# Optimization experiments

Measured on AMD Instinct MI355X. Metric: run time of the kernel, lower is better.

The kernel has to match this reference:

```python
import jax, jax.numpy as jnp
import numpy as np

H, W, V = 32, 64, 13
B, C_IN = 8, 256
RADIUS = 6371.0 * 1000.0
NUM_LAT = H + 2
_j = np.arange(1, NUM_LAT - 1, dtype=np.float64)
_LATS = (90.0 - _j * 180.0 / (NUM_LAT - 1)) * np.pi / 180.0  # [32] radians
PIXEL_X = jnp.asarray(2.0 * np.pi * RADIUS * np.cos(_LATS) / W, dtype=jnp.float32).reshape(1, 1, H, 1)
PIXEL_Y = np.float32(np.pi * RADIUS / (H + 1))
_DZ = np.array([50, 50, 50, 50, 50, 75, 100, 100, 100, 125, 112, 75, 75], dtype=np.float32)
PIXEL_Z = jnp.asarray(_DZ).reshape(1, V, 1, 1)
PRESSURE = jnp.asarray([50, 100, 150, 200, 250, 300, 400, 500, 600, 700, 850, 925, 1000], dtype=jnp.float32).reshape(1, V, 1, 1)
M_Z = jnp.asarray(np.tril(np.ones((V, V), dtype=np.float32)) * _DZ[None, :])  # lower-tri integration matrix
LAT_GRID = jnp.asarray(_LATS, dtype=jnp.float32).reshape(1, 1, H, 1)

OMEGA, L_V, R_GAS, C_P, R_D = 7.29e-5, 2.5e6, 8.314, 1005.0, 287.0
DIFF_RATIO, DT, K_H, K_V = 0.05, 300.0, 15.0, 0.1
SIGMA, EMIS, PTHRESH = 5.67e-8, 0.7, 0.8
sg = jax.lax.stop_gradient


def d_x(f):  # periodic 4th-order diff along W, kernel [1,-8,0,8,-1]/12
    g = (jnp.roll(f, 2, 3) - 8.0 * jnp.roll(f, 1, 3) + 8.0 * jnp.roll(f, -1, 3) - jnp.roll(f, -2, 3)) / 12.0
    return g / PIXEL_X


def d_y(f):  # replicate-block padding along H, kernel [-1,8,0,-8,1]/12
    p = jnp.concatenate([f[:, :, :2], f, f[:, :, -2:]], axis=2)
    g = (-p[:, :, :-4] + 8.0 * p[:, :, 1:-3] - 8.0 * p[:, :, 3:-1] + p[:, :, 4:]) / 12.0
    return g / PIXEL_Y


def d_z(f):  # replicate-block padding along level dim (axis 1)
    p = jnp.concatenate([f[:, :2], f, f[:, -2:]], axis=1)
    g = (-p[:, :-4] + 8.0 * p[:, 1:-3] - 8.0 * p[:, 3:-1] + p[:, 4:]) / 12.0
    return g / PIXEL_Z


def integral_z(f):
    return jnp.einsum('ij,bjhw->bihw', M_Z, f)


def conv3x3(x, w, b):
    y = jax.lax.conv_general_dilated(x, w, (1, 1), ((1, 1), (1, 1)), dimension_numbers=('NCHW', 'OIHW', 'NCHW'))
    return y + b[None, :, None, None]


def batchnorm(x, g, b, eps=1e-5):  # training-mode BN (batch statistics)
    m = x.mean(axis=(0, 2, 3), keepdims=True)
    v = x.var(axis=(0, 2, 3), keepdims=True)
    return (x - m) / jnp.sqrt(v + eps) * g.reshape(1, -1, 1, 1) + b.reshape(1, -1, 1, 1)


def scale_tensor(t, a, b):
    mn, mx = sg(t.min()), sg(t.max())
    return (t - mn) / (mx - mn) * (b - a) + a


def scale_diff(d, x):
    mn, me, mx = sg(x.min()), sg(x.mean()), sg(x.max())
    return scale_tensor(d, (mn - me) * DIFF_RATIO, (mx - me) * DIFF_RATIO)


def avoid_inf(t, thr=1.0):
    t = jnp.where(jnp.abs(t) == 0.0, jnp.full_like(t, 0.1), t)
    return jnp.where(jnp.abs(t) < thr, jnp.sign(t) * thr, t)


def mixing(f):
    return K_H * (d_x(d_x(f)) + d_y(d_y(f))) + K_V * d_z(d_z(f))


def rad_cool(t):
    ta = t + 273.15
    return -(EMIS * SIGMA * ta ** 4) / (C_P * PRESSURE * 100.0 / (R_D * ta))


def saturation(t, z_z):
    rho = -1.0 / avoid_inf(z_z)
    p = rho * R_GAS * t
    tc = t - 273.15
    e_s = 6.112 * jnp.exp(scale_tensor(17.67 * tc / avoid_inf(tc + 243.5), -3.47, 3.01)) * 100.0
    return jnp.maximum(0.622 * e_s / avoid_inf(p - 0.378 * e_s), 1e-6)


def precip(q, q_s):
    rh = q / avoid_inf(q_s)
    rate = (rh > PTHRESH).astype(q.dtype) * (q - PTHRESH * q_s) / DT
    return rate, rate * L_V / C_P


def uv_dt(u, v, w, u_x, v_y, z_x, z_y):
    # u_x, v_y are held fixed across RK stages (stateful self.u_x/self.v_y in the original)
    f_cor = 2.0 * OMEGA * jnp.sin(LAT_GRID)
    u_t = -u * u_x - v * d_y(u) - w * d_z(u) + f_cor * v - z_x + mixing(u)
    v_t = -u * d_x(v) - v * v_y - w * d_z(v) - f_cor * u - z_y + mixing(v)
    return u_t, v_t


def t_dt(u, v, w, t, q, q_s, z_z):
    Q = -L_V * z_z * w
    _, lh = precip(q, q_s)
    return (Q - z_z * w) / C_P - u * d_x(t) - v * d_y(t) - w * d_z(t) + mixing(t) + rad_cool(t) + lh


def pde_forward(x, w_norm, b_norm, w_innorm, b_innorm, coef, gz, bz, gq, bq, gu, bu, gv, bv, gt, bt, gblk, bblk):
    h = conv3x3(x, w_norm, b_norm)  # [B, 65, H, W]
    z, q, u, v, t = jnp.split(h, 5, axis=1)
    z = batchnorm(z, gz, bz); q = batchnorm(q, gq, bq)
    u = batchnorm(u, gu, bu); v = batchnorm(v, gv, bv); t = batchnorm(t, gt, bt)
    z_x, z_y, z_z = d_x(z), d_y(z), d_z(z)
    u_x, v_y = d_x(u), d_y(v)
    w_vel = -integral_z(u_x + v_y)  # continuity: dw/dz = -(u_x + v_y)
    # --- RK4 momentum evolution ---
    k1u, k1v = uv_dt(u, v, w_vel, u_x, v_y, z_x, z_y)
    k2u, k2v = uv_dt(u + 0.5 * DT * k1u, v + 0.5 * DT * k1v, w_vel, u_x, v_y, z_x, z_y)
    k3u, k3v = uv_dt(u + 0.5 * DT * k2u, v + 0.5 * DT * k2v, w_vel, u_x, v_y, z_x, z_y)
    k4u, k4v = uv_dt(u + DT * k3u, v + DT * k3v, w_vel, u_x, v_y, z_x, z_y)
    u_new = u + sg(scale_diff((k1u + 2 * k2u + 2 * k3u + k4u) / 6.0 * DT, u))
    v_new = v + sg(scale_diff((k1v + 2 * k2v + 2 * k3v + k4v) / 6.0 * DT, v))
    # --- RK4 temperature evolution (q_s fixed from initial t) ---
    q_s = saturation(t, z_z)
    k1t = t_dt(u, v, w_vel, t, q, q_s, z_z)
    k2t = t_dt(u, v, w_vel, t + 0.5 * DT * k1t, q, q_s, z_z)
    k3t = t_dt(u, v, w_vel, t + 0.5 * DT * k2t, q, q_s, z_z)
    k4t = t_dt(u, v, w_vel, t + DT * k3t, q, q_s, z_z)
    t_new = t + sg(scale_diff((k1t + 2 * k2t + 2 * k3t + k4t) / 6.0 * DT, t))
    # geopotential tendency uses stateful self.t_t (last computed stage = k4t)
    z_t = integral_z(-R_GAS / PRESSURE * k4t)
    z_new = z + sg(scale_diff(z_t * DT, z))
    # moisture evolution
    pr, _ = precip(q, q_s)
    q_t = -u * d_x(q) - v * d_y(q) - w_vel * d_z(q) + mixing(q) - pr
    q_new = q + sg(scale_diff(q_t * DT, q))
    phys = jnp.concatenate([z_new, q_new, u_new, v_new, t_new], axis=1)
    out = coef * phys + (1.0 - coef) * h
    out = conv3x3(out, w_innorm, b_innorm)
    return batchnorm(out, gblk, bblk) + x


def setup_inputs() -> dict:
    key = jax.random.key(0)
    k0, k1, k2 = jax.random.split(key, 3)
    VD = V * 5
    ones13 = jnp.ones((V,), jnp.float32)
    zeros13 = jnp.zeros((V,), jnp.float32)
    return {
        'x': jax.random.normal(k0, (B, C_IN, H, W), jnp.float32),
        'w_norm': jax.random.normal(k1, (VD, C_IN, 3, 3), jnp.float32) * 0.02,
        'b_norm': jnp.zeros((VD,), jnp.float32),
        'w_innorm': jax.random.normal(k2, (C_IN, VD, 3, 3), jnp.float32) * 0.02,
        'b_innorm': jnp.zeros((C_IN,), jnp.float32),
        'coef': 0.5 * jnp.ones((1, VD, H, W), jnp.float32),
        'gz': 0.1 * ones13, 'bz': zeros13,
        'gq': 0.1 * ones13, 'bq': zeros13,
        'gu': 0.1 * ones13, 'bu': zeros13,
        'gv': 0.1 * ones13, 'bv': zeros13,
        'gt': 0.1 * ones13, 'bt': zeros13,
        'gblk': jnp.ones((C_IN,), jnp.float32),
        'bblk': jnp.zeros((C_IN,), jnp.float32),
    }


def reference(x, w_norm, b_norm, w_innorm, b_innorm, coef, gz, bz, gq, bq, gu, bu, gv, bv, gt, bt, gblk, bblk):
    return pde_forward(x, w_norm, b_norm, w_innorm, b_innorm, coef, gz, bz, gq, bq, gu, bu, gv, bv, gt, bt, gblk, bblk)
```

## Files before the change

### kernel.cpp

```cpp
#include <hip/hip_runtime.h>
#include <math.h>

#define DEVFN static __device__ __forceinline__

static constexpr int BB = 8, VV = 13, HH = 32, WW = 64;
static constexpr int NPLANE = HH * WW;
static constexpr int NF = BB * VV * NPLANE;
static constexpr int NHB = BB * 65 * NPLANE;

static constexpr float DT = 300.0f;
static constexpr float KHc = 15.0f, KVc = 0.1f;
static constexpr float OMEGAc = 7.29e-5f;
static constexpr float L_Vc = 2.5e6f;
static constexpr float R_GASc = 8.314f;
static constexpr float C_Pc = 1005.0f;
static constexpr float PTHc = 0.8f;
static constexpr float PYc  = (float)(3.14159265358979323846 * 6371000.0 / 33.0);
static constexpr float PXCc = (float)(2.0 * 3.14159265358979323846 * 6371000.0 / 64.0);
static constexpr float RCCc = (float)(0.7 * 5.67e-8 * 287.0 / (1005.0 * 100.0));
static constexpr float FBIG = 3.402823466e38f;

__constant__ float cDZ[13]  = {50,50,50,50,50,75,100,100,100,125,112,75,75};
__constant__ float cPRS[13] = {50,100,150,200,250,300,400,500,600,700,850,925,1000};

typedef short bf16x8 __attribute__((ext_vector_type(8)));
typedef float f32x4 __attribute__((ext_vector_type(4)));

DEVFN int pmh(int r){ return r < 0 ? r + 2 : (r > HH - 1 ? r - 2 : r); }
DEVFN int pmv(int r){ return r < 0 ? r + 2 : (r > VV - 1 ? r - 2 : r); }
DEVFN float latOf(int h){ return (90.0f - (float)(h + 1) * (180.0f / 33.0f)) * 0.017453292519943295f; }
DEVFN float avoid_inf(float t){
  if (t == 0.0f) t = 0.1f;
  if (fabsf(t) < 1.0f) t = copysignf(1.0f, t);
  return t;
}
DEVFN unsigned short f2bf(float f){
  unsigned u = __float_as_uint(f);
  unsigned r = (u + 0x7fffu + ((u >> 16) & 1u)) >> 16;
  return (unsigned short)r;
}

DEVFN float d_xf(const float* __restrict__ F, int rb, int w, float invpx){
  return (F[rb + ((w + 62) & 63)] - 8.f * F[rb + ((w + 63) & 63)]
        + 8.f * F[rb + ((w + 1) & 63)] - F[rb + ((w + 2) & 63)]) * (1.f / 12.f) * invpx;
}
DEVFN float d_yf(const float* __restrict__ F, int bvbase, int h, int w){
  return (-F[bvbase + pmh(h - 2) * 64 + w] + 8.f * F[bvbase + pmh(h - 1) * 64 + w]
          - 8.f * F[bvbase + pmh(h + 1) * 64 + w] + F[bvbase + pmh(h + 2) * 64 + w]) * (1.f / 12.f) * (1.f / PYc);
}
DEVFN float d_zf(const float* __restrict__ F, int bbase, int v, int hw){
  return (-F[bbase + pmv(v - 2) * 2048 + hw] + 8.f * F[bbase + pmv(v - 1) * 2048 + hw]
          - 8.f * F[bbase + pmv(v + 1) * 2048 + hw] + F[bbase + pmv(v + 2) * 2048 + hw]) * (1.f / 12.f) / cDZ[v];
}
DEVFN float dxxf(const float* __restrict__ F, int rb, int w, float invpx){
  float s = F[rb + ((w + 60) & 63)] - 16.f * F[rb + ((w + 61) & 63)] + 64.f * F[rb + ((w + 62) & 63)]
          + 16.f * F[rb + ((w + 63) & 63)] - 130.f * F[rb + w] + 16.f * F[rb + ((w + 1) & 63)]
          + 64.f * F[rb + ((w + 2) & 63)] - 16.f * F[rb + ((w + 3) & 63)] + F[rb + ((w + 4) & 63)];
  return s * (1.f / 144.f) * invpx * invpx;
}
DEVFN float dyyf(const float* __restrict__ F, int bvbase, int h, int w){
  float g0 = d_yf(F, bvbase, pmh(h - 2), w);
  float g1 = d_yf(F, bvbase, pmh(h - 1), w);
  float g2 = d_yf(F, bvbase, pmh(h + 1), w);
  float g3 = d_yf(F, bvbase, pmh(h + 2), w);
  return (-g0 + 8.f * g1 - 8.f * g2 + g3) * (1.f / 12.f) * (1.f / PYc);
}
DEVFN float dzzf(const float* __restrict__ F, int bbase, int v, int hw){
  float g0 = d_zf(F, bbase, pmv(v - 2), hw);
  float g1 = d_zf(F, bbase, pmv(v - 1), hw);
  float g2 = d_zf(F, bbase, pmv(v + 1), hw);
  float g3 = d_zf(F, bbase, pmv(v + 2), hw);
  return (-g0 + 8.f * g1 - 8.f * g2 + g3) * (1.f / 12.f) / cDZ[v];
}

DEVFN float waveRedSum(float v){ for (int o = 32; o; o >>= 1) v += __shfl_down(v, o, 64); return v; }
DEVFN float waveRedMin(float v){ for (int o = 32; o; o >>= 1) v = fminf(v, __shfl_down(v, o, 64)); return v; }
DEVFN float waveRedMax(float v){ for (int o = 32; o; o >>= 1) v = fmaxf(v, __shfl_down(v, o, 64)); return v; }

template<int OP, int NWV>
static __device__ float blockRedN(float v){
  __shared__ float s[NWV];
  v = OP == 0 ? waveRedSum(v) : OP == 1 ? waveRedMin(v) : waveRedMax(v);
  int lane = threadIdx.x & 63, wid = threadIdx.x >> 6;
  __syncthreads();
  if (lane == 0) s[wid] = v;
  __syncthreads();
  float r = s[0];
  #pragma unroll
  for (int k = 1; k < NWV; ++k)
    r = OP == 0 ? r + s[k] : OP == 1 ? fminf(r, s[k]) : fmaxf(r, s[k]);
  return r;
}

struct GB { const float* g[5]; const float* b[5]; };

__global__ void __launch_bounds__(256) pre_k(const float* __restrict__ x,
    const float* __restrict__ w1, const float* __restrict__ w2,
    unsigned short* __restrict__ XT, unsigned short* __restrict__ wp1,
    unsigned short* __restrict__ wp2)
{
  int blk = blockIdx.x, t = threadIdx.x;
  if (blk < 1024){
    __shared__ float tile[16 * 68];
    int zz = blk >> 8, rem = blk & 255;
    int b = rem >> 5, h = rem & 31;
    for (int p = zz * 4; p < zz * 4 + 4; ++p){
      int cbase = p * 16;
      __syncthreads();
      {
        int cl = t >> 4, w4 = (t & 15) * 4;
        float4 v = *(const float4*)(x + (((size_t)(b * 256 + cbase + cl) * 32 + h) * 64 + w4));
        tile[cl * 68 + w4 + 0] = v.x; tile[cl * 68 + w4 + 1] = v.y;
        tile[cl * 68 + w4 + 2] = v.z; tile[cl * 68 + w4 + 3] = v.w;
      }
      __syncthreads();
      {
        int w = t >> 2, c4 = (t & 3) * 4;
        ushort4 o;
        o.x = f2bf(tile[(c4 + 0) * 68 + w]);
        o.y = f2bf(tile[(c4 + 1) * 68 + w]);
        o.z = f2bf(tile[(c4 + 2) * 68 + w]);
        o.w = f2bf(tile[(c4 + 3) * 68 + w]);
        *(ushort4*)(XT + (((size_t)(b * 32 + h) * 64 + w) * 256 + cbase + c4)) = o;
      }
    }
  } else {
    const int T1 = 9 * 80 * 256;
    const int T2 = 9 * 256 * 96;
    int idx = (blk - 1024) * 256 + t;
    if (idx < T1){
      int dir = idx / (80 * 256);
      int r = idx - dir * (80 * 256);
      int co = r / 256, ci = r - co * 256;
      float v = (co < 65) ? w1[((size_t)(co * 256 + ci)) * 9 + dir] : 0.f;
      wp1[idx] = f2bf(v);
    } else if (idx < T1 + T2){
      int j = idx - T1;
      int dir = j / (256 * 96);
      int r = j - dir * (256 * 96);
      int co = r / 96, ci = r - co * 96;
      float v = (ci < 65) ? w2[((size_t)(co * 65 + ci)) * 9 + dir] : 0.f;
      wp2[j] = f2bf(v);
    }
  }
}

template<int CIT, int CIL, int CO, int COp, int NW, int MF, int SWZ>
__global__ void __launch_bounds__(NW * 64) conv_mfma_k(
    const unsigned short* __restrict__ XT, const unsigned short* __restrict__ Wp,
    const float* __restrict__ bias, float* __restrict__ out, float* __restrict__ bnp)
{
  __shared__ __align__(16) unsigned short Xl[3 * 34 * CIL];
  const int C8 = CIL / 8;
  int tid = threadIdx.x;
// ... 102 lines not shown
        float g = gb.g[f][k], bbv = gb.b[f][k];
        As[ch] = g * rstd; Bs[ch] = bbv - m * g * rstd;
      }
    }
  }
  __syncthreads();

  int part = blk >> 6;
  int col = ((blk & 63) << 8) | t;
  int b = col >> 11, p = col & 2047, h = p >> 6, w = p & 63;
  int hbase = b * 65 * NPLANE;
  auto hn = [&](int ch, int hh, int ww)->float {
    return hb[hbase + ch * 2048 + hh * 64 + ww] * As[ch] + Bs[ch];
  };
  int fb = (b * 13) * 2048 + p;
  float lat = latOf(h);
  float invpx = 1.0f / (PXCc * cosf(lat));
  int wm2 = (w + 62) & 63, wm1 = (w + 63) & 63, wpl1 = (w + 1) & 63, wpl2 = (w + 2) & 63;
  int hm2 = pmh(h - 2), hm1 = pmh(h - 1), hp1 = pmh(h + 1), hp2 = pmh(h + 2);
  float fmn = FBIG, fmx = -FBIG, fsm = 0.f, smn = FBIG, smx = -FBIG;
  if (part < 5){
    int ch0 = part * 13;
    float c[13];
    #pragma unroll
    for (int v = 0; v < 13; ++v) c[v] = hn(ch0 + v, h, w);
    float* Fdst = part == 0 ? Fz : part == 1 ? Fq : part == 2 ? Fu : part == 3 ? Fvf : Ft;
    #pragma unroll
    for (int v = 0; v < 13; ++v) Fdst[fb + v * 2048] = c[v];
    if (part == 0){
      #pragma unroll
      for (int v = 0; v < 13; ++v){
        zz[fb + v * 2048] = (-c[pmv(v - 2)] + 8.f * c[pmv(v - 1)] - 8.f * c[pmv(v + 1)] + c[pmv(v + 2)]) * (1.f / 12.f) / cDZ[v];
        float zxv = (hn(v, h, wm2) - 8.f * hn(v, h, wm1) + 8.f * hn(v, h, wpl1) - hn(v, h, wpl2)) * (1.f / 12.f) * invpx;
        float zyv = (-hn(v, hm2, w) + 8.f * hn(v, hm1, w) - 8.f * hn(v, hp1, w) + hn(v, hp2, w)) * (1.f / 12.f) * (1.f / PYc);
        zx[fb + v * 2048] = zxv; zy[fb + v * 2048] = zyv;
      }
    }
    if (part == 2){
      #pragma unroll
      for (int v = 0; v < 13; ++v){
        float uxv = (hn(26 + v, h, wm2) - 8.f * hn(26 + v, h, wm1) + 8.f * hn(26 + v, h, wpl1) - hn(26 + v, h, wpl2)) * (1.f / 12.f) * invpx;
        ux[fb + v * 2048] = uxv;
      }
    }
    if (part == 3){
      #pragma unroll
      for (int v = 0; v < 13; ++v){
        float vyv = (-hn(39 + v, hm2, w) + 8.f * hn(39 + v, hm1, w) - 8.f * hn(39 + v, hp1, w) + hn(39 + v, hp2, w)) * (1.f / 12.f) * (1.f / PYc);
        vy[fb + v * 2048] = vyv;
      }
    }
    if (part == 4){
      #pragma unroll
      for (int v = 0; v < 13; ++v){
        float tcc = c[v] - 273.15f;
        float arg = 17.67f * tcc / avoid_inf(tcc + 243.5f);
        smn = fminf(smn, arg); smx = fmaxf(smx, arg);
      }
    }
    #pragma unroll
    for (int v = 0; v < 13; ++v){ fmn = fminf(fmn, c[v]); fmx = fmaxf(fmx, c[v]); fsm += c[v]; }
  } else {
    float cum = 0.f;
    #pragma unroll
    for (int v = 0; v < 13; ++v){
      float uxv = (hn(26 + v, h, wm2) - 8.f * hn(26 + v, h, wm1) + 8.f * hn(26 + v, h, wpl1) - hn(26 + v, h, wpl2)) * (1.f / 12.f) * invpx;
      float vyv = (-hn(39 + v, hm2, w) + 8.f * hn(39 + v, hm1, w) - 8.f * hn(39 + v, hp1, w) + hn(39 + v, hp2, w)) * (1.f / 12.f) * (1.f / PYc);
      cum += cDZ[v] * (uxv + vyv);
      wv[fb + v * 2048] = -cum;
    }
  }
  float* pb = partS + blk * 17;
  float r;
  r = blockRedN<1,4>(smn); if (!t) pb[0] = r;
  r = blockRedN<2,4>(smx); if (!t) pb[1] = r;
  #pragma unroll
  for (int f = 0; f < 5; ++f){
    r = blockRedN<1,4>(part == f ? fmn : FBIG);  if (!t) pb[2 + f * 3] = r;
    r = blockRedN<2,4>(part == f ? fmx : -FBIG); if (!t) pb[3 + f * 3] = r;
    r = blockRedN<0,4>(part == f ? fsm : 0.f);   if (!t) pb[4 + f * 3] = r;
  }
}

template<int STAGE>
__global__ void __launch_bounds__(256) stage_k(
  const float* U, const float* Vf, const float* T,
  const float* Fu, const float* Fvf, const float* Ft, const float* Fq,
  const float* ux, const float* vy, const float* zx, const float* zy,
  const float* wv, const float* zz, const float* partS,
  float* C0, float* prr,
  float* Uo, float* Vo, float* To,
  float* duA, float* dvA, float* dtA, float* k4t, float* qtA,
  float* pduv, float* pdt, float* pqt, float cnext)
{
  float ss = 0.f, off = 0.f;
  if (STAGE == 1){
    int tt = threadIdx.x;
    float v0 = partS[tt * 17], v1 = partS[tt * 17 + 1];
    if (tt < 128){
      v0 = fminf(v0, partS[(tt + 256) * 17]);
      v1 = fmaxf(v1, partS[(tt + 256) * 17 + 1]);
    }
    float smn = blockRedN<1,4>(v0);
    float smx = blockRedN<2,4>(v1);
    ss = (3.01f + 3.47f) / (smx - smn);
    off = -3.47f - smn * ss;
  }
  int i = blockIdx.x * 256 + threadIdx.x;
  int w = i & 63, h = (i >> 6) & 31;
  int bv = i >> 11;
  int v = bv % 13;
  int bvbase = bv * 2048;
  int rb = bvbase + h * 64;
  int bbase = (bv - v) * 2048;
  int hw = h * 64 + w;
  float lat = latOf(h);
  float invpx = 1.0f / (PXCc * cosf(lat));
  float fcor = 2.0f * OMEGAc * sinf(lat);
  float wvi = wv[i];
  float Ui = U[i], Vi = Vf[i], Ti = T[i];
  float Fui = (STAGE == 1) ? Ui : Fu[i];
  float Fvi = (STAGE == 1) ? Vi : Fvf[i];

  float dyU = d_yf(U, bvbase, h, w);
  float dzU = d_zf(U, bbase, v, hw);
  float dxV = d_xf(Vf, rb, w, invpx);
  float dzV = d_zf(Vf, bbase, v, hw);
  float mixU = KHc * (dxxf(U, rb, w, invpx) + dyyf(U, bvbase, h, w)) + KVc * dzzf(U, bbase, v, hw);
  float mixV = KHc * (dxxf(Vf, rb, w, invpx) + dyyf(Vf, bvbase, h, w)) + KVc * dzzf(Vf, bbase, v, hw);
  float ku = -Ui * ux[i] - Vi * dyU - wvi * dzU + fcor * Vi - zx[i] + mixU;
  float kv = -Ui * dxV - Vi * vy[i] - wvi * dzV - fcor * Ui - zy[i] + mixV;

  float C0i;
  if (STAGE == 1){
    float zzi = zz[i], qi = Fq[i];
    float rho = -1.0f / avoid_inf(zzi);
    float p = rho * R_GASc * Ti;
    float tcc = Ti - 273.15f;
    float arg = 17.67f * tcc / avoid_inf(tcc + 243.5f);
    float es = 6.112f * expf(arg * ss + off) * 100.0f;
    float qs = fmaxf(0.622f * es / avoid_inf(p - 0.378f * es), 1e-6f);
    float rh = qi / avoid_inf(qs);
    float rate = (rh > PTHc) ? (qi - PTHc * qs) * (1.0f / DT) : 0.0f;
    prr[i] = rate;
    C0i = -(L_Vc + 1.0f) * zzi * wvi * (1.0f / C_Pc) + rate * (L_Vc / C_Pc);
    C0[i] = C0i;
  } else {
    C0i = C0[i];
  }

  float dxT = d_xf(T, rb, w, invpx);
  float dyT = d_yf(T, bvbase, h, w);
  float dzT = d_zf(T, bbase, v, hw);
  float mixT = KHc * (dxxf(T, rb, w, invpx) + dyyf(T, bvbase, h, w)) + KVc * dzzf(T, bbase, v, hw);
  float ta = Ti + 273.15f;
  float t2 = ta * ta;
  float ta5 = t2 * t2 * ta;
  float rc = -RCCc * ta5 / cPRS[v];
  float kt = C0i - Fui * dxT - Fvi * dyT - wvi * dzT + mixT + rc;

  if (STAGE == 1){ duA[i] = ku; dvA[i] = kv; dtA[i] = kt; }
  else if (STAGE < 4){ duA[i] += 2.f * ku; dvA[i] += 2.f * kv; dtA[i] += 2.f * kt; }
  else {
    float au = duA[i] + ku, av = dvA[i] + kv, at = dtA[i] + kt;
    duA[i] = au; dvA[i] = av; dtA[i] = at; k4t[i] = kt;
    float m0 = blockRedN<1,4>(au), m1 = blockRedN<2,4>(au);
    float m2 = blockRedN<1,4>(av), m3 = blockRedN<2,4>(av);
    float m4 = blockRedN<1,4>(at), m5 = blockRedN<2,4>(at);
    if (!threadIdx.x){
      float* pp = pduv + blockIdx.x * 4;
      pp[0] = m0; pp[1] = m1; pp[2] = m2; pp[3] = m3;
      pdt[blockIdx.x * 2] = m4; pdt[blockIdx.x * 2 + 1] = m5;
    }
  }
  if (STAGE < 4){
    float Fti = (STAGE == 1) ? Ti : Ft[i];
    Uo[i] = Fui + cnext * ku;
    Vo[i] = Fvi + cnext * kv;
    To[i] = Fti + cnext * kt;
  }

  if (STAGE == 2){
    float qtv = -Fui * d_xf(Fq, rb, w, invpx) - Fvi * d_yf(Fq, bvbase, h, w) - wvi * d_zf(Fq, bbase, v, hw)
              + KHc * (dxxf(Fq, rb, w, invpx) + dyyf(Fq, bvbase, h, w)) + KVc * dzzf(Fq, bbase, v, hw) - prr[i];
    qtA[i] = qtv;
    float m0 = blockRedN<1,4>(qtv), m1 = blockRedN<2,4>(qtv);
    if (!threadIdx.x){ pqt[blockIdx.x * 2] = m0; pqt[blockIdx.x * 2 + 1] = m1; }
  }
}

__global__ void __launch_bounds__(64) zt_k(const float* __restrict__ k4t, float* __restrict__ zt, float* __restrict__ pmm)
{
  int col = blockIdx.x * 64 + threadIdx.x;
  int b = col >> 11, p = col & 2047;
  int fb = b * 13 * 2048 + p;
  float cum = 0.f, mn = FBIG, mx = -FBIG;
  #pragma unroll
  for (int v = 0; v < 13; ++v){
    cum += cDZ[v] * (-R_GASc / cPRS[v]) * k4t[fb + v * 2048];
    zt[fb + v * 2048] = cum;
    mn = fminf(mn, cum); mx = fmaxf(mx, cum);
  }
  mn = waveRedMin(mn); mx = waveRedMax(mx);
  if (!threadIdx.x){ pmm[blockIdx.x * 2] = mn; pmm[blockIdx.x * 2 + 1] = mx; }
}

__global__ void __launch_bounds__(256) outmid_fused_k(
  const float* __restrict__ hb,
  const float* __restrict__ Fz, const float* __restrict__ Fq, const float* __restrict__ Fu,
  const float* __restrict__ Fvf, const float* __restrict__ Ft,
  const float* __restrict__ ztA, const float* __restrict__ qtA,
  const float* __restrict__ duA, const float* __restrict__ dvA, const float* __restrict__ dtA,
  const float* __restrict__ coef, const float* __restrict__ partS,
  const float* __restrict__ pduv, const float* __restrict__ pdt,
  const float* __restrict__ pqt, const float* __restrict__ pzt,
  unsigned short* __restrict__ MT)
{
  __shared__ float tileBig[65 * 66];
  int blk = blockIdx.x, t = threadIdx.x;

  float fmn[5] = {FBIG, FBIG, FBIG, FBIG, FBIG};
  float fmx[5] = {-FBIG, -FBIG, -FBIG, -FBIG, -FBIG};
  float fsm[5] = {0.f, 0.f, 0.f, 0.f, 0.f};
  #pragma unroll 1
  for (int r0 = t; r0 < 384; r0 += 256){
    const float* pr = partS + r0 * 17;
    #pragma unroll
    for (int f = 0; f < 5; ++f){
      fmn[f] = fminf(fmn[f], pr[2 + f * 3]);
      fmx[f] = fmaxf(fmx[f], pr[3 + f * 3]);
      fsm[f] += pr[4 + f * 3];
    }
  }
  #pragma unroll
  for (int f = 0; f < 5; ++f){
    fmn[f] = blockRedN<1,4>(fmn[f]);
    fmx[f] = blockRedN<2,4>(fmx[f]);
    fsm[f] = blockRedN<0,4>(fsm[f]);
  }
  float dumn = FBIG, dumx = -FBIG, dvmn = FBIG, dvmx = -FBIG, dtmn = FBIG, dtmx = -FBIG;
  float qmn = FBIG, qmx = -FBIG;
  #pragma unroll 1
  for (int r0 = t; r0 < 832; r0 += 256){
    dumn = fminf(dumn, pduv[r0 * 4]);     dumx = fmaxf(dumx, pduv[r0 * 4 + 1]);
    dvmn = fminf(dvmn, pduv[r0 * 4 + 2]); dvmx = fmaxf(dvmx, pduv[r0 * 4 + 3]);
    dtmn = fminf(dtmn, pdt[r0 * 2]);      dtmx = fmaxf(dtmx, pdt[r0 * 2 + 1]);
    qmn = fminf(qmn, pqt[r0 * 2]);        qmx = fmaxf(qmx, pqt[r0 * 2 + 1]);
  }
  float zmn = pzt[t * 2], zmx = pzt[t * 2 + 1];
  dumn = blockRedN<1,4>(dumn); dumx = blockRedN<2,4>(dumx);
  dvmn = blockRedN<1,4>(dvmn); dvmx = blockRedN<2,4>(dvmx);
  dtmn = blockRedN<1,4>(dtmn); dtmx = blockRedN<2,4>(dtmx);
  qmn = blockRedN<1,4>(qmn);   qmx = blockRedN<2,4>(qmx);
  zmn = blockRedN<1,4>(zmn);   zmx = blockRedN<2,4>(zmx);

  float scf[5], off2[5];
  {
    float rmn[5] = {zmn, qmn, dumn, dvmn, dtmn};
    float rmx[5] = {zmx, qmx, dumx, dvmx, dtmx};
    float cfs[5] = {DT, DT, DT / 6.f, DT / 6.f, DT / 6.f};
    #pragma unroll
    for (int f = 0; f < 5; ++f){
      float mnf = fmn[f], mef = fsm[f] * (1.0f / (float)NF), mxf = fmx[f];
      float aa = (mnf - mef) * 0.05f, b2 = (mxf - mef) * 0.05f;
      float cf = cfs[f];
      float dmn = rmn[f] * cf, dmx = rmx[f] * cf;
      float s = (b2 - aa) / (dmx - dmn);
      scf[f] = s * cf; off2[f] = aa - dmn * s;
    }
  }

  int b = blk >> 5, h = blk & 31;
  #pragma unroll 1
  for (int idx = t; idx < 65 * 64; idx += 256){
    int c = idx >> 6, w = idx & 63;
    int f = c / 13, v = c - f * 13;
    int fi = (b * 13 + v) * 2048 + h * 64 + w;
    const float *Fp, *Rp;
    switch (f){
      case 0: Fp = Fz;  Rp = ztA; break;
      case 1: Fp = Fq;  Rp = qtA; break;
      case 2: Fp = Fu;  Rp = duA; break;
      case 3: Fp = Fvf; Rp = dvA; break;
      default: Fp = Ft; Rp = dtA; break;
    }
    float phys = Fp[fi] + Rp[fi] * scf[f] + off2[f];
    float cf = coef[c * 2048 + h * 64 + w];
    float hbv = hb[((size_t)(b * 65 + c)) * 2048 + h * 64 + w];
    tileBig[c * 66 + w] = cf * phys + (1.0f - cf) * hbv;
  }
  __syncthreads();
  #pragma unroll 1
  for (int ph = 0; ph < 6; ++ph){
    int cbase = ph * 16;
    int w = t >> 2, c4 = (t & 3) * 4;
    int c0 = cbase + c4;
    ushort4 o;
    o.x = (c0 + 0 < 65) ? f2bf(tileBig[(c0 + 0) * 66 + w]) : (unsigned short)0;
    o.y = (c0 + 1 < 65) ? f2bf(tileBig[(c0 + 1) * 66 + w]) : (unsigned short)0;
    o.z = (c0 + 2 < 65) ? f2bf(tileBig[(c0 + 2) * 66 + w]) : (unsigned short)0;
    o.w = (c0 + 3 < 65) ? f2bf(tileBig[(c0 + 3) * 66 + w]) : (unsigned short)0;
    *(ushort4*)(MT + (((size_t)(b * 32 + h) * 64 + w) * 96 + c0)) = o;
  }
}

__global__ void __launch_bounds__(256) final_k(float* __restrict__ y, const float* __restrict__ x,
  const float* __restrict__ bnp2, const float* __restrict__ gblk, const float* __restrict__ bblk)
{
  int blk = blockIdx.x, t = threadIdx.x;
  int c = (blk >> 1) & 255;
  float4 pv = ((const float4*)(bnp2 + (size_t)c * 1024))[t];
  float s = pv.x + pv.z, sq = pv.y + pv.w;
  s = blockRedN<0,4>(s); sq = blockRedN<0,4>(sq);
  float m = s * (1.0f / 16384.0f);
  float var = sq * (1.0f / 16384.0f) - m * m;
  float rstd = rsqrtf(var + 1e-5f);
  float a = gblk[c] * rstd, bb = bblk[c] - m * gblk[c] * rstd;
  int e4 = blk * 256 + t;
  float4 v = ((const float4*)y)[e4];
  float4 xv = ((const float4*)x)[e4];
  v.x = v.x * a + bb + xv.x;
  v.y = v.y * a + bb + xv.y;
  v.z = v.z * a + bb + xv.z;
  v.w = v.w * a + bb + xv.w;
  ((float4*)y)[e4] = v;
}

extern "C" void kernel_launch(void* const* d_in, const int* in_sizes, int n_in,
                              void* d_out, int out_size, void* d_ws, size_t ws_size,
                              hipStream_t stream)
{
  (void)in_sizes; (void)n_in; (void)out_size; (void)ws_size;
  const float* x        = (const float*)d_in[0];
  const float* w_norm   = (const float*)d_in[1];
  const float* b_norm   = (const float*)d_in[2];
  const float* w_innorm = (const float*)d_in[3];
  const float* b_innorm = (const float*)d_in[4];
  const float* coef     = (const float*)d_in[5];
  GB gb;
  for (int f = 0; f < 5; ++f){
    gb.g[f] = (const float*)d_in[6 + 2 * f];
    gb.b[f] = (const float*)d_in[7 + 2 * f];
  }
  const float* gblk = (const float*)d_in[16];
  const float* bblk = (const float*)d_in[17];
  float* yout = (float*)d_out;

  float* ws = (float*)d_ws;
  size_t off = 0;
  auto alloc = [&](size_t n){ float* p = ws + off; off += n; return p; };
  float* hb  = alloc(NHB);
  float* Fz  = alloc(NF); float* Fq  = alloc(NF); float* Fu  = alloc(NF);
  float* Fvf = alloc(NF); float* Ft  = alloc(NF);
  float* zx  = alloc(NF); float* zy  = alloc(NF); float* zz  = alloc(NF);
  float* ux  = alloc(NF); float* vy  = alloc(NF); float* wvel = alloc(NF);
  float* C0  = alloc(NF); float* prr = alloc(NF);
  float* Ua  = alloc(NF); float* Ub  = alloc(NF); float* Va  = alloc(NF); float* Vb = alloc(NF);
  float* Ta  = alloc(NF); float* Tb  = alloc(NF);
  float* duA = alloc(NF); float* dvA = alloc(NF); float* dtA = alloc(NF);
  float* k4t = alloc(NF); float* ztA = alloc(NF); float* qtA = alloc(NF);
  float* part1 = alloc(384 * 17 + 4);
  float* pduv = alloc(832 * 4); float* pdt = alloc(832 * 2);
  float* pqt  = alloc(832 * 2); float* pzt = alloc(256 * 2);
  float* bnp1 = alloc(65 * 512 * 2);
  float* bnp2 = alloc(256 * 512 * 2);
  float* Wp1f = alloc(9 * 80 * 256 / 2);
  float* Wp2f = alloc(9 * 256 * 96 / 2);
  unsigned short* Wp1 = (unsigned short*)Wp1f;
  unsigned short* Wp2 = (unsigned short*)Wp2f;
  unsigned short* XT = (unsigned short*)Ua;
  unsigned short* MT = (unsigned short*)C0;

  pre_k<<<2608, 256, 0, stream>>>(x, w_norm, w_innorm, XT, Wp1, Wp2);
  conv_mfma_k<256, 128, 65, 80, 5, 1, 7><<<dim3(64, 8), 5 * 64, 0, stream>>>(XT, Wp1, b_norm, hb, bnp1);
  prep_k<<<384, 256, 0, stream>>>(hb, bnp1, gb, Fz, Fq, Fu, Fvf, Ft, zx, zy, zz, ux, vy, wvel, part1);
  stage_k<1><<<NF / 256, 256, 0, stream>>>(Fu, Fvf, Ft, Fu, Fvf, Ft, Fq, ux, vy, zx, zy, wvel, zz, part1,
      C0, prr, Ua, Va, Ta, duA, dvA, dtA, k4t, qtA, pduv, pdt, pqt, 0.5f * DT);
  stage_k<2><<<NF / 256, 256, 0, stream>>>(Ua, Va, Ta, Fu, Fvf, Ft, Fq, ux, vy, zx, zy, wvel, zz, part1,
      C0, prr, Ub, Vb, Tb, duA, dvA, dtA, k4t, qtA, pduv, pdt, pqt, 0.5f * DT);
  stage_k<3><<<NF / 256, 256, 0, stream>>>(Ub, Vb, Tb, Fu, Fvf, Ft, Fq, ux, vy, zx, zy, wvel, zz, part1,
      C0, prr, Ua, Va, Ta, duA, dvA, dtA, k4t, qtA, pduv, pdt, pqt, DT);
  stage_k<4><<<NF / 256, 256, 0, stream>>>(Ua, Va, Ta, Fu, Fvf, Ft, Fq, ux, vy, zx, zy, wvel, zz, part1,
      C0, prr, Ub, Vb, Tb, duA, dvA, dtA, k4t, qtA, pduv, pdt, pqt, 0.f);
  zt_k<<<256, 64, 0, stream>>>(k4t, ztA, pzt);
  outmid_fused_k<<<256, 256, 0, stream>>>(hb, Fz, Fq, Fu, Fvf, Ft, ztA, qtA, duA, dvA, dtA,
      coef, part1, pduv, pdt, pqt, pzt, MT);
  conv_mfma_k<96, 96, 256, 256, 8, 2, 3><<<dim3(64, 8), 8 * 64, 0, stream>>>(MT, Wp2, b_innorm, yout, bnp2);
  final_k<<<4096, 256, 0, stream>>>(yout, x, bnp2, gblk, bblk);
}
```

Before: 181.2 us.

## Fuse RK4 stage pairs into halo-tiled kernels with LDS intermediate stages

```diff
diff --git a/kernel.cpp b/kernel.cpp
--- a/kernel.cpp
+++ b/kernel.cpp
@@ -70,6 +70,40 @@
   float g1 = d_zf(F, bbase, pmv(v - 1), hw);
   float g2 = d_zf(F, bbase, pmv(v + 1), hw);
   float g3 = d_zf(F, bbase, pmv(v + 2), hw);
+  return (-g0 + 8.f * g1 - 8.f * g2 + g3) * (1.f / 12.f) / cDZ[v];
+}
+
+#define SIDX(f,v,r,lw) (((f) * 13 + (v)) * 400 + (r) * 40 + (lw))
+DEVFN float dyL(const float* S, int f, int v, int gr, int lw, int ra0){
+  return (-S[SIDX(f, v, pmh(gr - 2) - ra0, lw)] + 8.f * S[SIDX(f, v, pmh(gr - 1) - ra0, lw)]
+          - 8.f * S[SIDX(f, v, pmh(gr + 1) - ra0, lw)] + S[SIDX(f, v, pmh(gr + 2) - ra0, lw)]) * (1.f / 12.f) * (1.f / PYc);
+}
+DEVFN float dzL(const float* S, int f, int v, int r, int lw){
+  return (-S[SIDX(f, pmv(v - 2), r, lw)] + 8.f * S[SIDX(f, pmv(v - 1), r, lw)]
+          - 8.f * S[SIDX(f, pmv(v + 1), r, lw)] + S[SIDX(f, pmv(v + 2), r, lw)]) * (1.f / 12.f) / cDZ[v];
+}
+DEVFN float dxL(const float* S, int f, int v, int r, int lw, float invpx){
+  int base = SIDX(f, v, r, lw);
+  return (S[base - 2] - 8.f * S[base - 1] + 8.f * S[base + 1] - S[base + 2]) * (1.f / 12.f) * invpx;
+}
+DEVFN float dxxL(const float* S, int f, int v, int r, int lw, float invpx){
+  int base = SIDX(f, v, r, lw);
+  float s = S[base - 4] - 16.f * S[base - 3] + 64.f * S[base - 2] + 16.f * S[base - 1] - 130.f * S[base]
+          + 16.f * S[base + 1] + 64.f * S[base + 2] - 16.f * S[base + 3] + S[base + 4];
+  return s * (1.f / 144.f) * invpx * invpx;
+}
+DEVFN float dyyL(const float* S, int f, int v, int gr, int lw, int ra0){
+  float g0 = dyL(S, f, v, pmh(gr - 2), lw, ra0);
+  float g1 = dyL(S, f, v, pmh(gr - 1), lw, ra0);
+  float g2 = dyL(S, f, v, pmh(gr + 1), lw, ra0);
+  float g3 = dyL(S, f, v, pmh(gr + 2), lw, ra0);
+  return (-g0 + 8.f * g1 - 8.f * g2 + g3) * (1.f / 12.f) * (1.f / PYc);
+}
+DEVFN float dzzL(const float* S, int f, int v, int r, int lw){
+  float g0 = dzL(S, f, pmv(v - 2), r, lw);
+  float g1 = dzL(S, f, pmv(v - 1), r, lw);
+  float g2 = dzL(S, f, pmv(v + 1), r, lw);
+  float g3 = dzL(S, f, pmv(v + 2), r, lw);
   return (-g0 + 8.f * g1 - 8.f * g2 + g3) * (1.f / 12.f) / cDZ[v];
 }
 
@@ -338,127 +372,214 @@
   }
 }
 
-template<int STAGE>
-__global__ void __launch_bounds__(256) stage_k(
-  const float* U, const float* Vf, const float* T,
-  const float* Fu, const float* Fvf, const float* Ft, const float* Fq,
-  const float* ux, const float* vy, const float* zx, const float* zy,
-  const float* wv, const float* zz, const float* partS,
-  float* C0, float* prr,
-  float* Uo, float* Vo, float* To,
-  float* duA, float* dvA, float* dtA, float* k4t, float* qtA,
-  float* pduv, float* pdt, float* pqt, float cnext)
+template<int PAIR>
+__global__ void __launch_bounds__(512) stpair_k(
+  const float* __restrict__ Au, const float* __restrict__ Av, const float* __restrict__ At,
+  const float* __restrict__ Fu, const float* __restrict__ Fvf, const float* __restrict__ Ft,
+  const float* __restrict__ Fq,
+  const float* __restrict__ ux, const float* __restrict__ vy,
+  const float* __restrict__ zx, const float* __restrict__ zy,
+  const float* __restrict__ wv, const float* __restrict__ zz,
+  const float* __restrict__ partS,
+  float* __restrict__ C0,
+  float* __restrict__ Uo, float* __restrict__ Vo, float* __restrict__ To,
+  float* __restrict__ duA, float* __restrict__ dvA, float* __restrict__ dtA,
+  float* __restrict__ qtA, float* __restrict__ ztA,
+  float* __restrict__ pduv, float* __restrict__ pdt, float* __restrict__ pqt,
+  float* __restrict__ pzt)
 {
+  __shared__ float S[3 * 13 * 400];
+  __shared__ float Sk4[13 * 2 * 32];
+  int blk = blockIdx.x, t = threadIdx.x;
+  int b = blk >> 5, t5 = blk & 31;
+  int h0 = (t5 & 15) << 1, w0 = (t5 >> 4) << 5;
+  int ra0 = h0 - 4; if (ra0 < 0) ra0 = 0;
+  int ra1 = h0 + 5; if (ra1 > 31) ra1 = 31;
+  int nra = ra1 - ra0 + 1;
+  int bbase = (b * 13) * 2048;
+
   float ss = 0.f, off = 0.f;
-  if (STAGE == 1){
-    int tt = threadIdx.x;
-    float v0 = partS[tt * 17], v1 = partS[tt * 17 + 1];
-    if (tt < 128){
-      v0 = fminf(v0, partS[(tt + 256) * 17]);
-      v1 = fmaxf(v1, partS[(tt + 256) * 17 + 1]);
-    }
-    float smn = blockRedN<1,4>(v0);
-    float smx = blockRedN<2,4>(v1);
+  if (PAIR == 0){
+    float v0 = (t < 384) ? partS[t * 17] : FBIG;
+    float v1 = (t < 384) ? partS[t * 17 + 1] : -FBIG;
+    float smn = blockRedN<1,8>(v0);
+    float smx = blockRedN<2,8>(v1);
     ss = (3.01f + 3.47f) / (smx - smn);
     off = -3.47f - smn * ss;
   }
-  int i = blockIdx.x * 256 + threadIdx.x;
-  int w = i & 63, h = (i >> 6) & 31;
-  int bv = i >> 11;
-  int v = bv % 13;
-  int bvbase = bv * 2048;
-  int rb = bvbase + h * 64;
-  int bbase = (bv - v) * 2048;
-  int hw = h * 64 + w;
-  float lat = latOf(h);
-  float invpx = 1.0f / (PXCc * cosf(lat));
-  float fcor = 2.0f * OMEGAc * sinf(lat);
-  float wvi = wv[i];
-  float Ui = U[i], Vi = Vf[i], Ti = T[i];
-  float Fui = (STAGE == 1) ? Ui : Fu[i];
-  float Fvi = (STAGE == 1) ? Vi : Fvf[i];
-
-  float dyU = d_yf(U, bvbase, h, w);
-  float dzU = d_zf(U, bbase, v, hw);
-  float dxV = d_xf(Vf, rb, w, invpx);
-  float dzV = d_zf(Vf, bbase, v, hw);
-  float mixU = KHc * (dxxf(U, rb, w, invpx) + dyyf(U, bvbase, h, w)) + KVc * dzzf(U, bbase, v, hw);
-  float mixV = KHc * (dxxf(Vf, rb, w, invpx) + dyyf(Vf, bvbase, h, w)) + KVc * dzzf(Vf, bbase, v, hw);
-  float ku = -Ui * ux[i] - Vi * dyU - wvi * dzU + fcor * Vi - zx[i] + mixU;
-  float kv = -Ui * dxV - Vi * vy[i] - wvi * dzV - fcor * Ui - zy[i] + mixV;
-
-  float C0i;
-  if (STAGE == 1){
-    float zzi = zz[i], qi = Fq[i];
-    float rho = -1.0f / avoid_inf(zzi);
-    float p = rho * R_GASc * Ti;
-    float tcc = Ti - 273.15f;
-    float arg = 17.67f * tcc / avoid_inf(tcc + 243.5f);
-    float es = 6.112f * expf(arg * ss + off) * 100.0f;
-    float qs = fmaxf(0.622f * es / avoid_inf(p - 0.378f * es), 1e-6f);
-    float rh = qi / avoid_inf(qs);
-    float rate = (rh > PTHc) ? (qi - PTHc * qs) * (1.0f / DT) : 0.0f;
-    prr[i] = rate;
-    C0i = -(L_Vc + 1.0f) * zzi * wvi * (1.0f / C_Pc) + rate * (L_Vc / C_Pc);
-    C0[i] = C0i;
+  const float ca = (PAIR == 0) ? 0.5f * DT : DT;
+
+  int nA = nra * 40 * 13;
+  #pragma unroll 1
+  for (int e = t; e < nA; e += 512){
+    int lw = e % 40;
+    int rr = (e / 40) % nra;
+    int v = e / (40 * nra);
+    int gr = ra0 + rr;
+    int gw = (w0 - 4 + lw) & 63;
+    int bvbase = (b * 13 + v) * 2048;
+    int rb = bvbase + gr * 64;
+    int hw = gr * 64 + gw;
+    int i = bvbase + hw;
+    float lat = latOf(gr);
+    float invpx = 1.0f / (PXCc * cosf(lat));
+    float fcor = 2.0f * OMEGAc * sinf(lat);
+    float wvi = wv[i];
+    float Ui = Au[i], Vi = Av[i], Ti = At[i];
+    float Fui = (PAIR == 0) ? Ui : Fu[i];
+    float Fvi = (PAIR == 0) ? Vi : Fvf[i];
+    float Fti = (PAIR == 0) ? Ti : Ft[i];
+
+    float dyU = d_yf(Au, bvbase, gr, gw);
+    float dzU = d_zf(Au, bbase, v, hw);
+    float dxV = d_xf(Av, rb, gw, invpx);
+    float dzV = d_zf(Av, bbase, v, hw);
+    float mixU = KHc * (dxxf(Au, rb, gw, invpx) + dyyf(Au, bvbase, gr, gw)) + KVc * dzzf(Au, bbase, v, hw);
+    float mixV = KHc * (dxxf(Av, rb, gw, invpx) + dyyf(Av, bvbase, gr, gw)) + KVc * dzzf(Av, bbase, v, hw);
+    float ku = -Ui * ux[i] - Vi * dyU - wvi * dzU + fcor * Vi - zx[i] + mixU;
+    float kv = -Ui * dxV - Vi * vy[i] - wvi * dzV - fcor * Ui - zy[i] + mixV;
+
+    float C0i;
+    if (PAIR == 0){
+      float zzi = zz[i], qi = Fq[i];
+      float rho = -1.0f / avoid_inf(zzi);
+      float p = rho * R_GASc * Ti;
+      float tcc = Ti - 273.15f;
+      float arg = 17.67f * tcc / avoid_inf(tcc + 243.5f);
+      float es = 6.112f * expf(arg * ss + off) * 100.0f;
+      float qs = fmaxf(0.622f * es / avoid_inf(p - 0.378f * es), 1e-6f);
+      float rh = qi / avoid_inf(qs);
+      float rate = (rh > PTHc) ? (qi - PTHc * qs) * (1.0f / DT) : 0.0f;
+      C0i = -(L_Vc + 1.0f) * zzi * wvi * (1.0f / C_Pc) + rate * (L_Vc / C_Pc);
+      if (gr >= h0 && gr <= h0 + 1 && lw >= 4 && lw <= 35) C0[i] = C0i;
+    } else {
+      C0i = C0[i];
+    }
+
+    float dxT = d_xf(At, rb, gw, invpx);
+    float dyT = d_yf(At, bvbase, gr, gw);
+    float dzT = d_zf(At, bbase, v, hw);
+    float mixT = KHc * (dxxf(At, rb, gw, invpx) + dyyf(At, bvbase, gr, gw)) + KVc * dzzf(At, bbase, v, hw);
+    float ta = Ti + 273.15f;
+    float t2 = ta * ta;
+    float ta5 = t2 * t2 * ta;
+    float rc = -RCCc * ta5 / cPRS[v];
+    float kt = C0i - Fui * dxT - Fvi * dyT - wvi * dzT + mixT + rc;
+
+    S[SIDX(0, v, rr, lw)] = Fui + ca * ku;
+    S[SIDX(1, v, rr, lw)] = Fvi + ca * kv;
+    S[SIDX(2, v, rr, lw)] = Fti + ca * kt;
+  }
+  __syncthreads();
+
+  float m0a = FBIG, m1a = -FBIG, m2a = FBIG, m3a = -FBIG, m4a = FBIG, m5a = -FBIG;
+  float qmn = FBIG, qmx = -FBIG;
+  #pragma unroll 1
+  for (int e = t; e < 832; e += 512){
+    int ww = e & 31;
+    int r2 = (e >> 5) & 1;
+    int v = e >> 6;
+    int gr = h0 + r2;
+    int lw = 4 + ww;
+    int r = gr - ra0;
+    int gw = w0 + ww;
+    int bvbase = (b * 13 + v) * 2048;
+    int rb = bvbase + gr * 64;
+    int hw = gr * 64 + gw;
+    int i = bvbase + hw;
+    float lat = latOf(gr);
+    float invpx = 1.0f / (PXCc * cosf(lat));
+    float fcor = 2.0f * OMEGAc * sinf(lat);
+    float wvi = wv[i];
+    float Ui = S[SIDX(0, v, r, lw)], Vi = S[SIDX(1, v, r, lw)], Ti = S[SIDX(2, v, r, lw)];
+    float Fui = Fu[i], Fvi = Fvf[i], Fti = Ft[i];
+
+    float dyU = dyL(S, 0, v, gr, lw, ra0);
+    float dzU = dzL(S, 0, v, r, lw);
+    float dxV = dxL(S, 1, v, r, lw, invpx);
+    float dzV = dzL(S, 1, v, r, lw);
+    float mixU = KHc * (dxxL(S, 0, v, r, lw, invpx) + dyyL(S, 0, v, gr, lw, ra0)) + KVc * dzzL(S, 0, v, r, lw);
+    float mixV = KHc * (dxxL(S, 1, v, r, lw, invpx) + dyyL(S, 1, v, gr, lw, ra0)) + KVc * dzzL(S, 1, v, r, lw);
+    float ku = -Ui * ux[i] - Vi * dyU - wvi * dzU + fcor * Vi - zx[i] + mixU;
+    float kv = -Ui * dxV - Vi * vy[i] - wvi * dzV - fcor * Ui - zy[i] + mixV;
+
+    float C0i = C0[i];
+    float dxT = dxL(S, 2, v, r, lw, invpx);
+    float dyT = dyL(S, 2, v, gr, lw, ra0);
+    float dzT = dzL(S, 2, v, r, lw);
+    float mixT = KHc * (dxxL(S, 2, v, r, lw, invpx) + dyyL(S, 2, v, gr, lw, ra0)) + KVc * dzzL(S, 2, v, r, lw);
+    float ta = Ti + 273.15f;
+    float t2 = ta * ta;
+    float ta5 = t2 * t2 * ta;
+    float rc = -RCCc * ta5 / cPRS[v];
+    float kt = C0i - Fui * dxT - Fvi * dyT - wvi * dzT + mixT + rc;
+
+    if (PAIR == 0){
+      float k1u = (Ui - Fui) * (2.0f / DT);
+      float k1v = (Vi - Fvi) * (2.0f / DT);
+      float k1t = (Ti - Fti) * (2.0f / DT);
+      duA[i] = k1u + 2.f * ku;
+      dvA[i] = k1v + 2.f * kv;
+      dtA[i] = k1t + 2.f * kt;
+      Uo[i] = Fui + 0.5f * DT * ku;
+      Vo[i] = Fvi + 0.5f * DT * kv;
+      To[i] = Fti + 0.5f * DT * kt;
+      float zzi = zz[i], qi = Fq[i];
+      float rho = -1.0f / avoid_inf(zzi);
+      float p = rho * R_GASc * Fti;
+      float tcc = Fti - 273.15f;
+      float arg = 17.67f * tcc / avoid_inf(tcc + 243.5f);
+      float es = 6.112f * expf(arg * ss + off) * 100.0f;
+      float qs = fmaxf(0.622f * es / avoid_inf(p - 0.378f * es), 1e-6f);
+      float rh = qi / avoid_inf(qs);
+      float rate = (rh > PTHc) ? (qi - PTHc * qs) * (1.0f / DT) : 0.0f;
+      float qtv = -Fui * d_xf(Fq, rb, gw, invpx) - Fvi * d_yf(Fq, bvbase, gr, gw) - wvi * d_zf(Fq, bbase, v, hw)
+                + KHc * (dxxf(Fq, rb, gw, invpx) + dyyf(Fq, bvbase, gr, gw)) + KVc * dzzf(Fq, bbase, v, hw) - rate;
+      qtA[i] = qtv;
+      qmn = fminf(qmn, qtv); qmx = fmaxf(qmx, qtv);
+    } else {
+      float k3u = (Ui - Fui) * (1.0f / DT);
+      float k3v = (Vi - Fvi) * (1.0f / DT);
+      float k3t = (Ti - Fti) * (1.0f / DT);
+      float au = duA[i] + 2.f * k3u + ku;
+      float av = dvA[i] + 2.f * k3v + kv;
+      float at = dtA[i] + 2.f * k3t + kt;
+      duA[i] = au; dvA[i] = av; dtA[i] = at;
+      Sk4[(v * 2 + r2) * 32 + ww] = kt;
+      m0a = fminf(m0a, au); m1a = fmaxf(m1a, au);
+      m2a = fminf(m2a, av); m3a = fmaxf(m3a, av);
+      m4a = fminf(m4a, at); m5a = fmaxf(m5a, at);
+    }
+  }
+
+  if (PAIR == 0){
+    float r0 = blockRedN<1,8>(qmn), r1 = blockRedN<2,8>(qmx);
+    if (!t){ pqt[blk * 2] = r0; pqt[blk * 2 + 1] = r1; }
   } else {
-    C0i = C0[i];
-  }
-
-  float dxT = d_xf(T, rb, w, invpx);
-  float dyT = d_yf(T, bvbase, h, w);
-  float dzT = d_zf(T, bbase, v, hw);
-  float mixT = KHc * (dxxf(T, rb, w, invpx) + dyyf(T, bvbase, h, w)) + KVc * dzzf(T, bbase, v, hw);
-  float ta = Ti + 273.15f;
-  float t2 = ta * ta;
-  float ta5 = t2 * t2 * ta;
-  float rc = -RCCc * ta5 / cPRS[v];
-  float kt = C0i - Fui * dxT - Fvi * dyT - wvi * dzT + mixT + rc;
-
-  if (STAGE == 1){ duA[i] = ku; dvA[i] = kv; dtA[i] = kt; }
-  else if (STAGE < 4){ duA[i] += 2.f * ku; dvA[i] += 2.f * kv; dtA[i] += 2.f * kt; }
-  else {
-    float au = duA[i] + ku, av = dvA[i] + kv, at = dtA[i] + kt;
-    duA[i] = au; dvA[i] = av; dtA[i] = at; k4t[i] = kt;
-    float m0 = blockRedN<1,4>(au), m1 = blockRedN<2,4>(au);
-    float m2 = blockRedN<1,4>(av), m3 = blockRedN<2,4>(av);
-    float m4 = blockRedN<1,4>(at), m5 = blockRedN<2,4>(at);
-    if (!threadIdx.x){
-      float* pp = pduv + blockIdx.x * 4;
-      pp[0] = m0; pp[1] = m1; pp[2] = m2; pp[3] = m3;
-      pdt[blockIdx.x * 2] = m4; pdt[blockIdx.x * 2 + 1] = m5;
-    }
-  }
-  if (STAGE < 4){
-    float Fti = (STAGE == 1) ? Ti : Ft[i];
-    Uo[i] = Fui + cnext * ku;
-    Vo[i] = Fvi + cnext * kv;
-    To[i] = Fti + cnext * kt;
-  }
-
-  if (STAGE == 2){
-    float qtv = -Fui * d_xf(Fq, rb, w, invpx) - Fvi * d_yf(Fq, bvbase, h, w) - wvi * d_zf(Fq, bbase, v, hw)
-              + KHc * (dxxf(Fq, rb, w, invpx) + dyyf(Fq, bvbase, h, w)) + KVc * dzzf(Fq, bbase, v, hw) - prr[i];
-    qtA[i] = qtv;
-    float m0 = blockRedN<1,4>(qtv), m1 = blockRedN<2,4>(qtv);
-    if (!threadIdx.x){ pqt[blockIdx.x * 2] = m0; pqt[blockIdx.x * 2 + 1] = m1; }
-  }
-}
-
-__global__ void __launch_bounds__(64) zt_k(const float* __restrict__ k4t, float* __restrict__ zt, float* __restrict__ pmm)
-{
-  int col = blockIdx.x * 64 + threadIdx.x;
-  int b = col >> 11, p = col & 2047;
-  int fb = b * 13 * 2048 + p;
-  float cum = 0.f, mn = FBIG, mx = -FBIG;
-  #pragma unroll
-  for (int v = 0; v < 13; ++v){
-    cum += cDZ[v] * (-R_GASc / cPRS[v]) * k4t[fb + v * 2048];
-    zt[fb + v * 2048] = cum;
-    mn = fminf(mn, cum); mx = fmaxf(mx, cum);
-  }
-  mn = waveRedMin(mn); mx = waveRedMax(mx);
-  if (!threadIdx.x){ pmm[blockIdx.x * 2] = mn; pmm[blockIdx.x * 2 + 1] = mx; }
+    float r0 = blockRedN<1,8>(m0a), r1 = blockRedN<2,8>(m1a);
+    float r2 = blockRedN<1,8>(m2a), r3 = blockRedN<2,8>(m3a);
+    float r4 = blockRedN<1,8>(m4a), r5 = blockRedN<2,8>(m5a);
+    if (!t){
+      float* pp = pduv + blk * 4;
+      pp[0] = r0; pp[1] = r1; pp[2] = r2; pp[3] = r3;
+      pdt[blk * 2] = r4; pdt[blk * 2 + 1] = r5;
+    }
+    __syncthreads();
+    if (t < 64){
+      int ww = t & 31, r2c = t >> 5;
+      int gr = h0 + r2c, gw = w0 + ww;
+      int fb = bbase + gr * 64 + gw;
+      float cum = 0.f, mn = FBIG, mx = -FBIG;
+      #pragma unroll
+      for (int v = 0; v < 13; ++v){
+        cum += cDZ[v] * (-R_GASc / cPRS[v]) * Sk4[(v * 2 + r2c) * 32 + ww];
+        ztA[fb + v * 2048] = cum;
+        mn = fminf(mn, cum); mx = fmaxf(mx, cum);
+      }
+      mn = waveRedMin(mn); mx = waveRedMax(mx);
+      if (!t){ pzt[blk * 2] = mn; pzt[blk * 2 + 1] = mx; }
+    }
+  }
 }
 
 __global__ void __launch_bounds__(256) outmid_fused_k(
@@ -494,16 +615,11 @@
     fmx[f] = blockRedN<2,4>(fmx[f]);
     fsm[f] = blockRedN<0,4>(fsm[f]);
   }
-  float dumn = FBIG, dumx = -FBIG, dvmn = FBIG, dvmx = -FBIG, dtmn = FBIG, dtmx = -FBIG;
-  float qmn = FBIG, qmx = -FBIG;
-  #pragma unroll 1
-  for (int r0 = t; r0 < 832; r0 += 256){
-    dumn = fminf(dumn, pduv[r0 * 4]);     dumx = fmaxf(dumx, pduv[r0 * 4 + 1]);
-    dvmn = fminf(dvmn, pduv[r0 * 4 + 2]); dvmx = fmaxf(dvmx, pduv[r0 * 4 + 3]);
-    dtmn = fminf(dtmn, pdt[r0 * 2]);      dtmx = fmaxf(dtmx, pdt[r0 * 2 + 1]);
-    qmn = fminf(qmn, pqt[r0 * 2]);        qmx = fmaxf(qmx, pqt[r0 * 2 + 1]);
-  }
-  float zmn = pzt[t * 2], zmx = pzt[t * 2 + 1];
+  float dumn = pduv[t * 4],     dumx = pduv[t * 4 + 1];
+  float dvmn = pduv[t * 4 + 2], dvmx = pduv[t * 4 + 3];
+  float dtmn = pdt[t * 2],      dtmx = pdt[t * 2 + 1];
+  float qmn = pqt[t * 2],       qmx = pqt[t * 2 + 1];
+  float zmn = pzt[t * 2],       zmx = pzt[t * 2 + 1];
   dumn = blockRedN<1,4>(dumn); dumx = blockRedN<2,4>(dumx);
   dvmn = blockRedN<1,4>(dvmn); dvmx = blockRedN<2,4>(dvmx);
   dtmn = blockRedN<1,4>(dtmn); dtmx = blockRedN<2,4>(dtmx);
@@ -614,31 +730,28 @@
   float* Ua  = alloc(NF); float* Ub  = alloc(NF); float* Va  = alloc(NF); float* Vb = alloc(NF);
   float* Ta  = alloc(NF); float* Tb  = alloc(NF);
   float* duA = alloc(NF); float* dvA = alloc(NF); float* dtA = alloc(NF);
-  float* k4t = alloc(NF); float* ztA = alloc(NF); float* qtA = alloc(NF);
+  float* k4t = alloc(NF);
+  float* ztA = alloc(NF); float* qtA = alloc(NF);
   float* part1 = alloc(384 * 17 + 4);
-  float* pduv = alloc(832 * 4); float* pdt = alloc(832 * 2);
-  float* pqt  = alloc(832 * 2); float* pzt = alloc(256 * 2);
+  float* pduv = alloc(256 * 4); float* pdt = alloc(256 * 2);
+  float* pqt  = alloc(256 * 2); float* pzt = alloc(256 * 2);
   float* bnp1 = alloc(65 * 512 * 2);
   float* bnp2 = alloc(256 * 512 * 2);
   float* Wp1f = alloc(9 * 80 * 256 / 2);
   float* Wp2f = alloc(9 * 256 * 96 / 2);
   unsigned short* Wp1 = (unsigned short*)Wp1f;
   unsigned short* Wp2 = (unsigned short*)Wp2f;
+  (void)prr; (void)k4t; (void)Ua; (void)Va; (void)Ta;
   unsigned short* XT = (unsigned short*)Ua;
   unsigned short* MT = (unsigned short*)C0;
 
   pre_k<<<2608, 256, 0, stream>>>(x, w_norm, w_innorm, XT, Wp1, Wp2);
   conv_mfma_k<256, 128, 65, 80, 5, 1, 7><<<dim3(64, 8), 5 * 64, 0, stream>>>(XT, Wp1, b_norm, hb, bnp1);
   prep_k<<<384, 256, 0, stream>>>(hb, bnp1, gb, Fz, Fq, Fu, Fvf, Ft, zx, zy, zz, ux, vy, wvel, part1);
-  stage_k<1><<<NF / 256, 256, 0, stream>>>(Fu, Fvf, Ft, Fu, Fvf, Ft, Fq, ux, vy, zx, zy, wvel, zz, part1,
-      C0, prr, Ua, Va, Ta, duA, dvA, dtA, k4t, qtA, pduv, pdt, pqt, 0.5f * DT);
-  stage_k<2><<<NF / 256, 256, 0, stream>>>(Ua, Va, Ta, Fu, Fvf, Ft, Fq, ux, vy, zx, zy, wvel, zz, part1,
-      C0, prr, Ub, Vb, Tb, duA, dvA, dtA, k4t, qtA, pduv, pdt, pqt, 0.5f * DT);
-  stage_k<3><<<NF / 256, 256, 0, stream>>>(Ub, Vb, Tb, Fu, Fvf, Ft, Fq, ux, vy, zx, zy, wvel, zz, part1,
-      C0, prr, Ua, Va, Ta, duA, dvA, dtA, k4t, qtA, pduv, pdt, pqt, DT);
-  stage_k<4><<<NF / 256, 256, 0, stream>>>(Ua, Va, Ta, Fu, Fvf, Ft, Fq, ux, vy, zx, zy, wvel, zz, part1,
-      C0, prr, Ub, Vb, Tb, duA, dvA, dtA, k4t, qtA, pduv, pdt, pqt, 0.f);
-  zt_k<<<256, 64, 0, stream>>>(k4t, ztA, pzt);
+  stpair_k<0><<<256, 512, 0, stream>>>(Fu, Fvf, Ft, Fu, Fvf, Ft, Fq, ux, vy, zx, zy, wvel, zz, part1,
+      C0, Ub, Vb, Tb, duA, dvA, dtA, qtA, ztA, pduv, pdt, pqt, pzt);
+  stpair_k<1><<<256, 512, 0, stream>>>(Ub, Vb, Tb, Fu, Fvf, Ft, Fq, ux, vy, zx, zy, wvel, zz, part1,
+      C0, Ub, Vb, Tb, duA, dvA, dtA, qtA, ztA, pduv, pdt, pqt, pzt);
   outmid_fused_k<<<256, 256, 0, stream>>>(hb, Fz, Fq, Fu, Fvf, Ft, ztA, qtA, duA, dvA, dtA,
       coef, part1, pduv, pdt, pqt, pzt, MT);
   conv_mfma_k<96, 96, 256, 256, 8, 2, 3><<<dim3(64, 8), 8 * 64, 0, stream>>>(MT, Wp2, b_innorm, yout, bnp2);
```

Result: slower. 387.7 us (+113.9%).
